# Kernel tuning notes

Measured on AMD Instinct MI355X. Metric: run time of the kernel, lower is better.

## Reference

```python
import jax, jax.numpy as jnp
import numpy as np

T, D = 8192, 256   # frames, feature dim
P, K = 64, 128     # phone vocabulary, centers per phone


def setup_inputs() -> dict:
    key = jax.random.key(0)
    k1, k2, k3 = jax.random.split(key, 3)
    h = jax.random.normal(k1, (T, D), dtype=jnp.float32)
    centers = jax.random.normal(k2, (P, K, D), dtype=jnp.float32)
    phones = jax.random.randint(k3, (T,), 0, P, dtype=jnp.int64)
    return {"h": h, "centers": centers, "phones": phones}


def reference(h, centers, phones):
    """Per-phone 1-NN retrieval: for each frame t, find nearest center in the
    pool for phones[t] and return that center (anonymized feature).
    centers: [P, K, D] padded table replacing the (pattern, phone, gender) dict.
    """
    c = centers[phones]                                # [T, K, D] irregular gather
    # squared euclidean distance; ||h_t||^2 is constant per row -> omit for argmin
    d2 = jnp.sum(c * c, axis=-1) - 2.0 * jnp.einsum("td,tkd->tk", h, c)  # [T, K]
    idx = jnp.argmin(d2, axis=-1)                      # [T]
    h_anon = jnp.take_along_axis(c, idx[:, None, None], axis=1)[:, 0, :]  # [T, D]
    return h_anon
```

## Files before the change

kernel.cpp:

```cpp
#include <hip/hip_runtime.h>

#define T_FRAMES 8192
#define D_DIM    256
#define P_PHONES 64
#define K_CENT   128
#define TILE_F   32
#define BUCKET_CAP 256
#define SLOTS_PP   8
#define MAX_SLOTS  (P_PHONES * SLOTS_PP)
#define MARGIN   1.0f

#define WS_NORMS  0
#define WS_FIDX   32768
#define WS_DESC   98304
#define WS_HH     106496
#define WS_CH     (106496 + 4194304)

typedef _Float16 half8 __attribute__((ext_vector_type(8)));
typedef float    f32x4 __attribute__((ext_vector_type(4)));

__global__ __launch_bounds__(1024) void qr_prep_kernel(const float* __restrict__ h,
                                                       const float* __restrict__ centers,
                                                       const int* __restrict__ phones,
                                                       float* __restrict__ norms,
                                                       int* __restrict__ fidx,
                                                       int4* __restrict__ desc,
                                                       _Float16* __restrict__ hH,
                                                       _Float16* __restrict__ cH) {
    const int b   = blockIdx.x;
    const int tid = threadIdx.x;

    if (b < 512) {
        const size_t e = ((size_t)b * 1024 + tid) * 4;
        union { _Float16 hf[4]; uint2 u; } pk;
        float4 v = *(const float4*)(h + e);
        pk.hf[0] = (_Float16)v.x; pk.hf[1] = (_Float16)v.y;
        pk.hf[2] = (_Float16)v.z; pk.hf[3] = (_Float16)v.w;
        *(uint2*)(hH + e) = pk.u;
        v = *(const float4*)(centers + e);
        pk.hf[0] = (_Float16)v.x; pk.hf[1] = (_Float16)v.y;
        pk.hf[2] = (_Float16)v.z; pk.hf[3] = (_Float16)v.w;
        *(uint2*)(cH + e) = pk.u;
        float s = v.x * v.x + v.y * v.y + v.z * v.z + v.w * v.w;
#pragma unroll
        for (int off = 32; off; off >>= 1) s += __shfl_xor(s, off, 64);
        if ((tid & 63) == 0) norms[b * 16 + (tid >> 6)] = s;
        return;
    }

    __shared__ int nsh;
    const int j    = b - 512;
    const int w    = tid >> 6;
    const int lane = tid & 63;
    if (tid == 0) nsh = 0;
    __syncthreads();

    for (int ch = 0; ch < 8; ++ch) {
        const int f = w * 512 + ch * 64 + lane;
        const bool mt = (phones[f] == j);
        const unsigned long long mask = __ballot(mt);
        const int cnt = __popcll(mask);
        int base = 0;
        if (cnt) {
            if (lane == 0) base = atomicAdd(&nsh, cnt);
            base = __shfl(base, 0, 64);
            if (mt) {
                const int pos = base + __popcll(mask & ((1ull << lane) - 1ull));
                if (pos < BUCKET_CAP) fidx[j * BUCKET_CAP + pos] = f;
            }
        }
    }
    __syncthreads();

    if (tid == 0) {
        const int c = nsh > BUCKET_CAP ? BUCKET_CAP : nsh;
#pragma unroll
        for (int k = 0; k < SLOTS_PP; ++k) {
            const int rem = c - k * TILE_F;
            const int fc  = rem < 0 ? 0 : (rem > TILE_F ? TILE_F : rem);
            desc[j * SLOTS_PP + k] = make_int4(j, j * BUCKET_CAP + k * TILE_F, fc, 0);
        }
    }
}

__global__ __launch_bounds__(256) void qr_main_kernel(const float* __restrict__ h,
                                                      const float* __restrict__ centers,
                                                      const float* __restrict__ norms,
                                                      const int* __restrict__ fidx,
                                                      const int4* __restrict__ desc,
                                                      const _Float16* __restrict__ hH,
                                                      const _Float16* __restrict__ cH,
                                                      float* __restrict__ out) {
    __shared__ float d2s[TILE_F * K_CENT];
    __shared__ float mins[TILE_F];
    __shared__ int   cnt[TILE_F];
    __shared__ short cand[TILE_F * 32];
    __shared__ int   widx[TILE_F];
    __shared__ int   rlist[TILE_F];
    __shared__ int   rn;

    const int4 dsc = desc[blockIdx.x];
    const int fcnt = dsc.z;
    if (fcnt == 0) return;
    const int p = dsc.x, fstart = dsc.y;

    const int tid  = threadIdx.x;
    const int wave = tid >> 6;
    const int lane = tid & 63;
    const int m    = lane & 15;
    const int quad = lane >> 4;

    if (tid < TILE_F) cnt[tid] = 0;
    if (tid == 0) rn = 0;

    half8 aF[2][8];
#pragma unroll
    for (int t = 0; t < 2; ++t) {
        const int fiA = fidx[fstart + min(t * 16 + m, fcnt - 1)];
        const _Float16* ap = hH + (size_t)fiA * D_DIM + quad * 8;
#pragma unroll
        for (int s = 0; s < 8; ++s) aF[t][s] = *(const half8*)(ap + s * 32);
    }

#pragma unroll
    for (int u = 0; u < 2; ++u) {
        const int c = (wave * 2 + u) * 16 + m;
        const _Float16* bp = cH + ((size_t)p * K_CENT + c) * D_DIM + quad * 8;
        half8 bF[8];
#pragma unroll
        for (int s = 0; s < 8; ++s) bF[s] = *(const half8*)(bp + s * 32);
        f32x4 acc0 = {0.f, 0.f, 0.f, 0.f};
        f32x4 acc1 = {0.f, 0.f, 0.f, 0.f};
#pragma unroll
        for (int s = 0; s < 8; ++s) {
            acc0 = __builtin_amdgcn_mfma_f32_16x16x32_f16(aF[0][s], bF[s], acc0, 0, 0, 0);
            acc1 = __builtin_amdgcn_mfma_f32_16x16x32_f16(aF[1][s], bF[s], acc1, 0, 0, 0);
        }
        const float nrm = norms[p * K_CENT + c];
#pragma unroll
        for (int r = 0; r < 4; ++r) {
            d2s[(quad * 4 + r) * K_CENT + c]        = nrm - 2.0f * acc0[r];
            d2s[(16 + quad * 4 + r) * K_CENT + c]   = nrm - 2.0f * acc1[r];
        }
    }
    __syncthreads();

    const int fr = tid >> 3;
    const int g  = tid & 7;
    float v[16];
    {
        float mn = 3.0e38f;
#pragma unroll
        for (int jx = 0; jx < 16; ++jx) {
            v[jx] = d2s[fr * K_CENT + g * 16 + jx];
            mn = fminf(mn, v[jx]);
        }
        mn = fminf(mn, __shfl_xor(mn, 1, 64));
        mn = fminf(mn, __shfl_xor(mn, 2, 64));
        mn = fminf(mn, __shfl_xor(mn, 4, 64));
        if (g == 0) mins[fr] = mn;
    }
    __syncthreads();

    {
        const float tau = mins[fr] + MARGIN;
#pragma unroll
        for (int jx = 0; jx < 16; ++jx) {
            if (v[jx] < tau) {
                const int pos = atomicAdd(&cnt[fr], 1);
                if (pos < 32) cand[fr * 32 + pos] = (short)(g * 16 + jx);
            }
        }
    }
    __syncthreads();

    if (tid < TILE_F && tid < fcnt) {
        if (cnt[tid] == 1) widx[tid] = (int)cand[tid * 32];
        else rlist[atomicAdd(&rn, 1)] = tid;
    }
    __syncthreads();

    for (int r = wave; r < rn; r += 4) {
        const int f2 = rlist[r];
        const int fi = fidx[fstart + f2];
        const float4 hv = ((const float4*)(h + (size_t)fi * D_DIM))[lane];
        const int n = cnt[f2];
        const int ncand = (n <= 32) ? n : K_CENT;
        float best = 3.0e38f; int bc = 0x7FFFFFFF;
        for (int ci = 0; ci < ncand; ++ci) {
            const int c = (n <= 32) ? (int)cand[f2 * 32 + ci] : ci;
            const float4 cv = ((const float4*)(centers + ((size_t)p * K_CENT + c) * D_DIM))[lane];
            float s = hv.x * cv.x + hv.y * cv.y + hv.z * cv.z + hv.w * cv.w;
#pragma unroll
            for (int off = 32; off; off >>= 1) s += __shfl_xor(s, off, 64);
            const float d2 = norms[p * K_CENT + c] - 2.0f * s;
            if (d2 < best || (d2 == best && c < bc)) { best = d2; bc = c; }
        }
        if (lane == 0) widx[f2] = bc;
    }
    __syncthreads();

    if (fr < fcnt) {
        const int fo = fidx[fstart + fr];
        const float4* src = (const float4*)(centers + ((size_t)p * K_CENT + widx[fr]) * D_DIM);
        float4* dst = (float4*)(out + (size_t)fo * D_DIM);
#pragma unroll
        for (int jx = 0; jx < 8; ++jx) dst[g + 8 * jx] = src[g + 8 * jx];
    }
}

extern "C" void kernel_launch(void* const* d_in, const int* in_sizes, int n_in,
                              void* d_out, int out_size, void* d_ws, size_t ws_size,
                              hipStream_t stream) {
    const float* h       = (const float*)d_in[0];
    const float* centers = (const float*)d_in[1];
    const int*   phones  = (const int*)d_in[2];
    float*       out     = (float*)d_out;

    char* ws = (char*)d_ws;
    float*     norms = (float*)(ws + WS_NORMS);
    int*       fidx  = (int*)(ws + WS_FIDX);
    int4*      desc  = (int4*)(ws + WS_DESC);
    _Float16*  hH    = (_Float16*)(ws + WS_HH);
    _Float16*  cH    = (_Float16*)(ws + WS_CH);

    qr_prep_kernel<<<576, 1024, 0, stream>>>(h, centers, phones, norms, fidx, desc, hH, cH);
    qr_main_kernel<<<MAX_SLOTS, 256, 0, stream>>>(h, centers, norms, fidx, desc, hH, cH, out);
}
```

Baseline: 87.58 us.

## Drop h fp16 prepass, make each wave own a 16-frame tile with register-only argmin

The prep kernel no longer converts h to fp16. The main kernel now loads h in fp32 and converts it to fp16 in registers, folding the -2 scale into the A fragment, and starts the MFMA accumulators at the center norms. Each wave handles one 16-frame slot and keeps all 128 distances in registers, so the shared-memory d2 tile, the block barriers and the atomics are gone and the argmin is done with shuffles. The exact fp32 fallback now scans all 128 centers per ambiguous frame instead of only the candidate list. That makes fallback frames more expensive but keeps the flow simpler, and the smaller tile gives more waves across the grid.

```diff
diff --git a/kernel.cpp b/kernel.cpp
--- a/kernel.cpp
+++ b/kernel.cpp
@@ -4,64 +4,59 @@
 #define D_DIM    256
 #define P_PHONES 64
 #define K_CENT   128
-#define TILE_F   32
+#define TILE_F   16
 #define BUCKET_CAP 256
-#define SLOTS_PP   8
-#define MAX_SLOTS  (P_PHONES * SLOTS_PP)
+#define SLOTS_PP   16
 #define MARGIN   1.0f
 
 #define WS_NORMS  0
 #define WS_FIDX   32768
 #define WS_DESC   98304
-#define WS_HH     106496
-#define WS_CH     (106496 + 4194304)
+#define WS_CH     131072
 
 typedef _Float16 half8 __attribute__((ext_vector_type(8)));
 typedef float    f32x4 __attribute__((ext_vector_type(4)));
 
-__global__ __launch_bounds__(1024) void qr_prep_kernel(const float* __restrict__ h,
-                                                       const float* __restrict__ centers,
+__global__ __launch_bounds__(1024) void qr_prep_kernel(const float* __restrict__ centers,
                                                        const int* __restrict__ phones,
                                                        float* __restrict__ norms,
                                                        int* __restrict__ fidx,
                                                        int4* __restrict__ desc,
-                                                       _Float16* __restrict__ hH,
                                                        _Float16* __restrict__ cH) {
-    const int b   = blockIdx.x;
-    const int tid = threadIdx.x;
-
-    if (b < 512) {
-        const size_t e = ((size_t)b * 1024 + tid) * 4;
-        union { _Float16 hf[4]; uint2 u; } pk;
-        float4 v = *(const float4*)(h + e);
-        pk.hf[0] = (_Float16)v.x; pk.hf[1] = (_Float16)v.y;
-        pk.hf[2] = (_Float16)v.z; pk.hf[3] = (_Float16)v.w;
-        *(uint2*)(hH + e) = pk.u;
-        v = *(const float4*)(centers + e);
-        pk.hf[0] = (_Float16)v.x; pk.hf[1] = (_Float16)v.y;
-        pk.hf[2] = (_Float16)v.z; pk.hf[3] = (_Float16)v.w;
-        *(uint2*)(cH + e) = pk.u;
-        float s = v.x * v.x + v.y * v.y + v.z * v.z + v.w * v.w;
-#pragma unroll
-        for (int off = 32; off; off >>= 1) s += __shfl_xor(s, off, 64);
-        if ((tid & 63) == 0) norms[b * 16 + (tid >> 6)] = s;
-        return;
-    }
-
-    __shared__ int nsh;
-    const int j    = b - 512;
+    const int b    = blockIdx.x;
+    const int tid  = threadIdx.x;
     const int w    = tid >> 6;
     const int lane = tid & 63;
+
+    if (b < 128) {
+#pragma unroll
+        for (int k = 0; k < 4; ++k) {
+            const size_t e = (size_t)b * 16384 + (size_t)k * 4096 + (size_t)tid * 4;
+            const float4 v = *(const float4*)(centers + e);
+            union { _Float16 hf[4]; uint2 u; } pk;
+            pk.hf[0] = (_Float16)v.x; pk.hf[1] = (_Float16)v.y;
+            pk.hf[2] = (_Float16)v.z; pk.hf[3] = (_Float16)v.w;
+            *(uint2*)(cH + e) = pk.u;
+            float s = v.x * v.x + v.y * v.y + v.z * v.z + v.w * v.w;
+#pragma unroll
+            for (int off = 32; off; off >>= 1) s += __shfl_xor(s, off, 64);
+            if (lane == 0) norms[b * 64 + k * 16 + w] = s;
+        }
+        return;
+    }
+
+    __shared__ int nsh;
+    const int j = b - 128;
     if (tid == 0) nsh = 0;
     __syncthreads();
-
+#pragma unroll
     for (int ch = 0; ch < 8; ++ch) {
         const int f = w * 512 + ch * 64 + lane;
         const bool mt = (phones[f] == j);
         const unsigned long long mask = __ballot(mt);
         const int cnt = __popcll(mask);
-        int base = 0;
         if (cnt) {
+            int base = 0;
             if (lane == 0) base = atomicAdd(&nsh, cnt);
             base = __shfl(base, 0, 64);
             if (mt) {
@@ -71,7 +66,6 @@
         }
     }
     __syncthreads();
-
     if (tid == 0) {
         const int c = nsh > BUCKET_CAP ? BUCKET_CAP : nsh;
 #pragma unroll
@@ -88,124 +82,119 @@
                                                       const float* __restrict__ norms,
                                                       const int* __restrict__ fidx,
                                                       const int4* __restrict__ desc,
-                                                      const _Float16* __restrict__ hH,
                                                       const _Float16* __restrict__ cH,
                                                       float* __restrict__ out) {
-    __shared__ float d2s[TILE_F * K_CENT];
-    __shared__ float mins[TILE_F];
-    __shared__ int   cnt[TILE_F];
-    __shared__ short cand[TILE_F * 32];
-    __shared__ int   widx[TILE_F];
-    __shared__ int   rlist[TILE_F];
-    __shared__ int   rn;
-
-    const int4 dsc = desc[blockIdx.x];
-    const int fcnt = dsc.z;
-    if (fcnt == 0) return;
-    const int p = dsc.x, fstart = dsc.y;
-
     const int tid  = threadIdx.x;
     const int wave = tid >> 6;
     const int lane = tid & 63;
     const int m    = lane & 15;
     const int quad = lane >> 4;
 
-    if (tid < TILE_F) cnt[tid] = 0;
-    if (tid == 0) rn = 0;
-
-    half8 aF[2][8];
-#pragma unroll
-    for (int t = 0; t < 2; ++t) {
-        const int fiA = fidx[fstart + min(t * 16 + m, fcnt - 1)];
-        const _Float16* ap = hH + (size_t)fiA * D_DIM + quad * 8;
-#pragma unroll
-        for (int s = 0; s < 8; ++s) aF[t][s] = *(const half8*)(ap + s * 32);
-    }
-
-#pragma unroll
-    for (int u = 0; u < 2; ++u) {
-        const int c = (wave * 2 + u) * 16 + m;
-        const _Float16* bp = cH + ((size_t)p * K_CENT + c) * D_DIM + quad * 8;
-        half8 bF[8];
-#pragma unroll
-        for (int s = 0; s < 8; ++s) bF[s] = *(const half8*)(bp + s * 32);
-        f32x4 acc0 = {0.f, 0.f, 0.f, 0.f};
-        f32x4 acc1 = {0.f, 0.f, 0.f, 0.f};
+    const int slot = ((blockIdx.x & 63) << 4) + ((blockIdx.x >> 6) << 2) + wave;
+    const int4 dsc = desc[slot];
+    const int fcnt = dsc.z;
+    if (fcnt == 0) return;
+    const int p = dsc.x, fstart = dsc.y;
+
+    const int fiA = fidx[fstart + min(m, fcnt - 1)];
+
+    half8 aF[8];
+    {
+        const float* ap = h + (size_t)fiA * D_DIM + quad * 8;
 #pragma unroll
         for (int s = 0; s < 8; ++s) {
-            acc0 = __builtin_amdgcn_mfma_f32_16x16x32_f16(aF[0][s], bF[s], acc0, 0, 0, 0);
-            acc1 = __builtin_amdgcn_mfma_f32_16x16x32_f16(aF[1][s], bF[s], acc1, 0, 0, 0);
-        }
-        const float nrm = norms[p * K_CENT + c];
-#pragma unroll
-        for (int r = 0; r < 4; ++r) {
-            d2s[(quad * 4 + r) * K_CENT + c]        = nrm - 2.0f * acc0[r];
-            d2s[(16 + quad * 4 + r) * K_CENT + c]   = nrm - 2.0f * acc1[r];
-        }
-    }
-    __syncthreads();
-
-    const int fr = tid >> 3;
-    const int g  = tid & 7;
-    float v[16];
-    {
-        float mn = 3.0e38f;
-#pragma unroll
-        for (int jx = 0; jx < 16; ++jx) {
-            v[jx] = d2s[fr * K_CENT + g * 16 + jx];
-            mn = fminf(mn, v[jx]);
-        }
-        mn = fminf(mn, __shfl_xor(mn, 1, 64));
-        mn = fminf(mn, __shfl_xor(mn, 2, 64));
-        mn = fminf(mn, __shfl_xor(mn, 4, 64));
-        if (g == 0) mins[fr] = mn;
-    }
-    __syncthreads();
-
-    {
-        const float tau = mins[fr] + MARGIN;
-#pragma unroll
-        for (int jx = 0; jx < 16; ++jx) {
-            if (v[jx] < tau) {
-                const int pos = atomicAdd(&cnt[fr], 1);
-                if (pos < 32) cand[fr * 32 + pos] = (short)(g * 16 + jx);
+            const float4 lo = *(const float4*)(ap + s * 32);
+            const float4 hi = *(const float4*)(ap + s * 32 + 4);
+            half8 t;
+            t[0] = (_Float16)(-2.f * lo.x); t[1] = (_Float16)(-2.f * lo.y);
+            t[2] = (_Float16)(-2.f * lo.z); t[3] = (_Float16)(-2.f * lo.w);
+            t[4] = (_Float16)(-2.f * hi.x); t[5] = (_Float16)(-2.f * hi.y);
+            t[6] = (_Float16)(-2.f * hi.z); t[7] = (_Float16)(-2.f * hi.w);
+            aF[s] = t;
+        }
+    }
+
+    f32x4 acc[8];
+#pragma unroll
+    for (int ch = 0; ch < 8; ++ch) {
+        const float nrm = norms[(p << 7) + ch * 16 + m];
+        f32x4 a = {nrm, nrm, nrm, nrm};
+        acc[ch] = a;
+    }
+    const _Float16* bpbase = cH + (((size_t)(p << 7) + m) << 8) + quad * 8;
+#pragma unroll
+    for (int s = 0; s < 8; ++s) {
+#pragma unroll
+        for (int ch = 0; ch < 8; ++ch) {
+            const half8 bF = *(const half8*)(bpbase + (size_t)ch * 4096 + s * 32);
+            acc[ch] = __builtin_amdgcn_mfma_f32_16x16x32_f16(aF[s], bF, acc[ch], 0, 0, 0);
+        }
+    }
+
+    int  wreg[4];
+    int  wcopy  = 0;
+    bool anyNeg = false;
+#pragma unroll
+    for (int r = 0; r < 4; ++r) {
+        float mn = fminf(fminf(fminf(acc[0][r], acc[1][r]), fminf(acc[2][r], acc[3][r])),
+                         fminf(fminf(acc[4][r], acc[5][r]), fminf(acc[6][r], acc[7][r])));
+#pragma unroll
+        for (int off = 1; off <= 8; off <<= 1) mn = fminf(mn, __shfl_xor(mn, off, 64));
+        const float tau = mn + MARGIN;
+        int cnt = 0, cand = 0x7FFFFFFF;
+#pragma unroll
+        for (int ch = 0; ch < 8; ++ch) {
+            if (acc[ch][r] < tau) { ++cnt; cand = min(cand, ch * 16 + m); }
+        }
+#pragma unroll
+        for (int off = 1; off <= 8; off <<= 1) {
+            cnt += __shfl_xor(cnt, off, 64);
+            cand = min(cand, __shfl_xor(cand, off, 64));
+        }
+        const int wr = (cnt == 1) ? cand : -1;
+        wreg[r] = wr;
+        anyNeg |= (wr < 0);
+        if (((lane >> 2) & 3) == r) wcopy = wr;
+    }
+
+    if (__any(anyNeg)) {
+#pragma unroll
+        for (int f = 0; f < TILE_F; ++f) {
+            const int wf = __shfl(wreg[f & 3], (f >> 2) << 4, 64);
+            if (wf >= 0 || f >= fcnt) continue;
+            const int fiF = __shfl(fiA, f, 64);
+            const float4* hp  = (const float4*)(h + (size_t)fiF * D_DIM);
+            const float4* cp0 = (const float4*)(centers + ((size_t)(p << 7) + lane) * D_DIM);
+            float s0 = 0.f, s1 = 0.f;
+#pragma unroll 4
+            for (int jx = 0; jx < 64; ++jx) {
+                const float4 a  = hp[jx];
+                const float4 b0 = cp0[jx];
+                const float4 b1 = cp0[jx + 64 * 64];
+                s0 += a.x * b0.x + a.y * b0.y + a.z * b0.z + a.w * b0.w;
+                s1 += a.x * b1.x + a.y * b1.y + a.z * b1.z + a.w * b1.w;
             }
-        }
-    }
-    __syncthreads();
-
-    if (tid < TILE_F && tid < fcnt) {
-        if (cnt[tid] == 1) widx[tid] = (int)cand[tid * 32];
-        else rlist[atomicAdd(&rn, 1)] = tid;
-    }
-    __syncthreads();
-
-    for (int r = wave; r < rn; r += 4) {
-        const int f2 = rlist[r];
-        const int fi = fidx[fstart + f2];
-        const float4 hv = ((const float4*)(h + (size_t)fi * D_DIM))[lane];
-        const int n = cnt[f2];
-        const int ncand = (n <= 32) ? n : K_CENT;
-        float best = 3.0e38f; int bc = 0x7FFFFFFF;
-        for (int ci = 0; ci < ncand; ++ci) {
-            const int c = (n <= 32) ? (int)cand[f2 * 32 + ci] : ci;
-            const float4 cv = ((const float4*)(centers + ((size_t)p * K_CENT + c) * D_DIM))[lane];
-            float s = hv.x * cv.x + hv.y * cv.y + hv.z * cv.z + hv.w * cv.w;
-#pragma unroll
-            for (int off = 32; off; off >>= 1) s += __shfl_xor(s, off, 64);
-            const float d2 = norms[p * K_CENT + c] - 2.0f * s;
-            if (d2 < best || (d2 == best && c < bc)) { best = d2; bc = c; }
-        }
-        if (lane == 0) widx[f2] = bc;
-    }
-    __syncthreads();
-
+            float best = norms[(p << 7) + lane] - 2.f * s0;
+            int   bc   = lane;
+            const float d1 = norms[(p << 7) + lane + 64] - 2.f * s1;
+            if (d1 < best) { best = d1; bc = lane + 64; }
+#pragma unroll
+            for (int off = 1; off < 64; off <<= 1) {
+                const float ob = __shfl_xor(best, off, 64);
+                const int   oc = __shfl_xor(bc, off, 64);
+                if (ob < best || (ob == best && oc < bc)) { best = ob; bc = oc; }
+            }
+            if ((lane >> 2) == f) wcopy = bc;
+        }
+    }
+
+    const int fr = lane >> 2, part = lane & 3;
     if (fr < fcnt) {
-        const int fo = fidx[fstart + fr];
-        const float4* src = (const float4*)(centers + ((size_t)p * K_CENT + widx[fr]) * D_DIM);
-        float4* dst = (float4*)(out + (size_t)fo * D_DIM);
-#pragma unroll
-        for (int jx = 0; jx < 8; ++jx) dst[g + 8 * jx] = src[g + 8 * jx];
+        const int fo = __shfl(fiA, fr, 64);
+        const float4* src = (const float4*)(centers + ((size_t)(p << 7) + wcopy) * D_DIM) + part;
+        float4*       dst = (float4*)(out + (size_t)fo * D_DIM) + part;
+#pragma unroll
+        for (int jx = 0; jx < 16; ++jx) dst[4 * jx] = src[4 * jx];
     }
 }
 
@@ -218,12 +207,11 @@
     float*       out     = (float*)d_out;
 
     char* ws = (char*)d_ws;
-    float*     norms = (float*)(ws + WS_NORMS);
-    int*       fidx  = (int*)(ws + WS_FIDX);
-    int4*      desc  = (int4*)(ws + WS_DESC);
-    _Float16*  hH    = (_Float16*)(ws + WS_HH);
-    _Float16*  cH    = (_Float16*)(ws + WS_CH);
-
-    qr_prep_kernel<<<576, 1024, 0, stream>>>(h, centers, phones, norms, fidx, desc, hH, cH);
-    qr_main_kernel<<<MAX_SLOTS, 256, 0, stream>>>(h, centers, norms, fidx, desc, hH, cH, out);
+    float*    norms = (float*)(ws + WS_NORMS);
+    int*      fidx  = (int*)(ws + WS_FIDX);
+    int4*     desc  = (int4*)(ws + WS_DESC);
+    _Float16* cH    = (_Float16*)(ws + WS_CH);
+
+    qr_prep_kernel<<<192, 1024, 0, stream>>>(centers, phones, norms, fidx, desc, cH);
+    qr_main_kernel<<<P_PHONES * 4, 256, 0, stream>>>(h, centers, norms, fidx, desc, cH, out);
 }
```

Measured after the change: 135.8 us. +55.1%, slower.
